# Kernel tuning notes

Hardware: AMD Instinct MI355X
Metric: run time of the kernel (lower is better)

The kernel has to match this reference:

```python
import jax, jax.numpy as jnp
import numpy as np

B, N, M, C = 8, 76725, 32, 12  # N = 9 anchors x (80^2+40^2+20^2+10^2+5^2) for a 640x640 image, P3-P7
IMG = 640.0


def setup_inputs() -> dict:
    key = jax.random.key(0)
    ks = jax.random.split(key, 7)
    # logits biased toward prior_prob~0.01 like the head's bias init
    cls_logits = jax.random.normal(ks[0], (B, N, C), jnp.float32) - 4.0
    box_deltas = 0.1 * jax.random.normal(ks[1], (B, N, 4), jnp.float32)
    # plausible anchors: random centers in image, sizes 16..256
    a_xy = jax.random.uniform(ks[2], (N, 2), jnp.float32) * IMG
    a_wh = 16.0 + jax.random.uniform(ks[3], (N, 2), jnp.float32) * 240.0
    anchors = jnp.concatenate([a_xy - 0.5 * a_wh, a_xy + 0.5 * a_wh], axis=-1)
    # padded ground truth: M boxes per image, all valid
    g_xy = jax.random.uniform(ks[4], (B, M, 2), jnp.float32) * (IMG - 96.0)
    g_wh = 16.0 + jax.random.uniform(ks[5], (B, M, 2), jnp.float32) * 80.0
    gt_boxes = jnp.concatenate([g_xy, g_xy + g_wh], axis=-1)
    gt_labels = jax.random.randint(ks[6], (B, M), 0, C)
    gt_valid = jnp.ones((B, M), dtype=bool)
    return {"cls_logits": cls_logits, "box_deltas": box_deltas, "anchors": anchors,
            "gt_boxes": gt_boxes, "gt_labels": gt_labels, "gt_valid": gt_valid}


def _box_iou(anchors, gt_boxes):
    # anchors [N,4], gt_boxes [B,M,4] -> [B,N,M]
    ax1, ay1, ax2, ay2 = (anchors[:, i] for i in range(4))
    gx1, gy1, gx2, gy2 = (gt_boxes[..., i] for i in range(4))
    iw = jnp.clip(jnp.minimum(ax2[None, :, None], gx2[:, None, :])
                  - jnp.maximum(ax1[None, :, None], gx1[:, None, :]), 0.0)
    ih = jnp.clip(jnp.minimum(ay2[None, :, None], gy2[:, None, :])
                  - jnp.maximum(ay1[None, :, None], gy1[:, None, :]), 0.0)
    inter = iw * ih
    area_a = (ax2 - ax1) * (ay2 - ay1)            # [N]
    area_g = (gx2 - gx1) * (gy2 - gy1)            # [B,M]
    union = area_a[None, :, None] + area_g[:, None, :] - inter
    return inter / union


def _encode_boxes(anchors, matched):
    aw = anchors[:, 2] - anchors[:, 0]
    ah = anchors[:, 3] - anchors[:, 1]
    acx = anchors[:, 0] + 0.5 * aw
    acy = anchors[:, 1] + 0.5 * ah
    gw = matched[..., 2] - matched[..., 0]
    gh = matched[..., 3] - matched[..., 1]
    gcx = matched[..., 0] + 0.5 * gw
    gcy = matched[..., 1] + 0.5 * gh
    return jnp.stack([(gcx - acx) / aw, (gcy - acy) / ah,
                      jnp.log(gw / aw), jnp.log(gh / ah)], axis=-1)


def reference(cls_logits, box_deltas, anchors, gt_boxes, gt_labels, gt_valid):
    # --- anchor assignment (box_iou + max over GT) ---
    ious = _box_iou(anchors, gt_boxes)                       # [B,N,M]
    ious = jnp.where(gt_valid[:, None, :], ious, -1.0)
    iou_max = ious.max(axis=-1)                              # [B,N]
    idx = ious.argmax(axis=-1)                               # [B,N]
    pos = iou_max >= 0.5
    valid = pos | (iou_max < 0.4)                            # non-ignore anchors
    matched = jnp.take_along_axis(
        gt_boxes, jnp.broadcast_to(idx[:, :, None], (B, N, 4)), axis=1)  # [B,N,4]
    mlab = jnp.take_along_axis(gt_labels, idx, axis=1)       # [B,N]
    f32 = cls_logits.dtype
    cls_t = jax.nn.one_hot(mlab, C, dtype=f32) * pos[..., None].astype(f32)
    # --- sigmoid focal loss (alpha=0.25, gamma=2), mean over non-ignored elements ---
    p = jax.nn.sigmoid(cls_logits)
    ce = -(cls_t * jax.nn.log_sigmoid(cls_logits)
           + (1.0 - cls_t) * jax.nn.log_sigmoid(-cls_logits))
    pt = cls_t * p + (1.0 - cls_t) * (1.0 - p)
    alpha_t = cls_t * 0.25 + (1.0 - cls_t) * 0.75
    focal = alpha_t * (1.0 - pt) ** 2 * ce                   # [B,N,C]
    vw = valid.astype(f32)
    cls_loss = jnp.sum(focal * vw[..., None]) / jnp.maximum(jnp.sum(vw) * C, 1.0)
    # --- smooth L1 (beta=1) on positives, mean over selected elements ---
    box_t = _encode_boxes(anchors, matched)                  # [B,N,4]
    d = jnp.abs(box_deltas - box_t)
    sl1 = jnp.where(d < 1.0, 0.5 * d * d, d - 0.5)
    pw = pos.astype(f32)
    box_loss = jnp.sum(sl1 * pw[..., None]) / jnp.maximum(jnp.sum(pw) * 4.0, 1.0)
    return cls_loss + box_loss
```

## Files before the change

### kernel.cpp

```cpp
#include <hip/hip_runtime.h>
#include <math.h>

#define NB 8
#define NA 76725
#define NM 32
#define NC 12
#define BLK 256
#define GX  128
#define NBLOCKS (GX * NB)


__global__ __launch_bounds__(BLK) void retina_fused(
    const float* __restrict__ cls_logits,
    const float* __restrict__ box_deltas,
    const float* __restrict__ anchors,
    const float* __restrict__ gt_boxes,
    const int* __restrict__ gt_labels,
    char* __restrict__ ws,
    int nslots, int slot_stride,
    unsigned int* __restrict__ cnt,
    float* __restrict__ out)
{
    __shared__ float4 s_gt[NM];
    __shared__ float  s_area[NM];
    __shared__ int    s_lab[NM];
    __shared__ int    s_islast;
    __shared__ double s_acc[64][4];

    const int b   = blockIdx.y;
    const int tid = threadIdx.x;

    if (tid < NM) {
        float4 g = ((const float4*)gt_boxes)[b * NM + tid];
        s_gt[tid]   = g;
        s_area[tid] = (g.z - g.x) * (g.w - g.y);
        s_lab[tid]  = gt_labels[b * NM + tid];
    }
    __syncthreads();

    float fsum = 0.0f;
    float ssum = 0.0f;
    int   vcnt = 0;
    int   pcnt = 0;

    for (int n0 = blockIdx.x * BLK; n0 < NA; n0 += GX * BLK) {
        const int n = n0 + tid;
        if (n >= NA) break;

        const float4 a = ((const float4*)anchors)[n];
        const float area_a = (a.z - a.x) * (a.w - a.y);

        float b_inter, b_uni;
        int   bidx = 0;
        {
            const float4 g = s_gt[0];
            const float iw = fmaxf(fminf(a.z, g.z) - fmaxf(a.x, g.x), 0.0f);
            const float ih = fmaxf(fminf(a.w, g.w) - fmaxf(a.y, g.y), 0.0f);
            b_inter = iw * ih;
            b_uni   = (area_a + s_area[0]) - b_inter;
        }
        #pragma unroll
        for (int m = 1; m < NM; ++m) {
            const float4 g = s_gt[m];
            const float iw = fmaxf(fminf(a.z, g.z) - fmaxf(a.x, g.x), 0.0f);
            const float ih = fmaxf(fminf(a.w, g.w) - fmaxf(a.y, g.y), 0.0f);
            const float inter = iw * ih;
            const float uni   = (area_a + s_area[m]) - inter;
            const bool gt = inter * b_uni > b_inter * uni;
            b_inter = gt ? inter : b_inter;
            b_uni   = gt ? uni   : b_uni;
            bidx    = gt ? m     : bidx;
        }

        const bool pos   = (b_inter >= 0.5f * b_uni);
        const bool valid = pos || (b_inter < 0.4f * b_uni);
        vcnt += valid ? 1 : 0;
        pcnt += pos ? 1 : 0;

        if (valid) {
            const int lab = pos ? s_lab[bidx] : -1;
            const float4* cl =
                (const float4*)(cls_logits + ((size_t)b * NA + n) * NC);
            float x[NC];
            const float4 c0 = cl[0], c1 = cl[1], c2 = cl[2];
            x[0]=c0.x; x[1]=c0.y; x[2]=c0.z; x[3]=c0.w;
            x[4]=c1.x; x[5]=c1.y; x[6]=c1.z; x[7]=c1.w;
            x[8]=c2.x; x[9]=c2.y; x[10]=c2.z; x[11]=c2.w;
            #pragma unroll
            for (int c = 0; c < NC; ++c) {
                const float xx = x[c];
                const float ax = fabsf(xx);
                const float e  = __expf(-ax);
                const float t  = 1.0f + e;
                const float l1pe = __logf(t);
                const float u  = __builtin_amdgcn_rcpf(t);
                const float v  = e * u;
                const bool xpos = (xx >= 0.0f);
                const float sp_mx = l1pe + fmaxf(-xx, 0.0f);
                const float sp_px = l1pe + fmaxf(xx, 0.0f);
                const bool tgt = (c == lab);
                const float q = tgt ? (xpos ? v : u) : (xpos ? u : v);
                const float s = tgt ? sp_mx : sp_px;
                const float al = tgt ? 0.25f : 0.75f;
                fsum += al * q * q * s;
            }
        }

        if (pos) {
            const float4 g = s_gt[bidx];
            const float aw  = a.z - a.x;
            const float ah  = a.w - a.y;
            const float r_aw = __builtin_amdgcn_rcpf(aw);
            const float r_ah = __builtin_amdgcn_rcpf(ah);
            const float acx = a.x + 0.5f * aw;
            const float acy = a.y + 0.5f * ah;
            const float gw  = g.z - g.x;
            const float gh  = g.w - g.y;
            const float gcx = g.x + 0.5f * gw;
            const float gcy = g.y + 0.5f * gh;
            const float t0 = (gcx - acx) * r_aw;
            const float t1 = (gcy - acy) * r_ah;
            const float t2 = __logf(gw * r_aw);
            const float t3 = __logf(gh * r_ah);
            const float4 d4 =
                ((const float4*)box_deltas)[(size_t)b * NA + n];
            float d;
            d = fabsf(d4.x - t0); ssum += (d < 1.0f) ? 0.5f * d * d : d - 0.5f;
            d = fabsf(d4.y - t1); ssum += (d < 1.0f) ? 0.5f * d * d : d - 0.5f;
            d = fabsf(d4.z - t2); ssum += (d < 1.0f) ? 0.5f * d * d : d - 0.5f;
            d = fabsf(d4.w - t3); ssum += (d < 1.0f) ? 0.5f * d * d : d - 0.5f;
        }
    }

    float4 v = make_float4(fsum, ssum, (float)vcnt, (float)pcnt);
    #pragma unroll
    for (int off = 32; off > 0; off >>= 1) {
        v.x += __shfl_down(v.x, off);
        v.y += __shfl_down(v.y, off);
        v.z += __shfl_down(v.z, off);
        v.w += __shfl_down(v.w, off);
    }
    __shared__ float4 s_red[BLK / 64];
    const int wave = tid >> 6;
    const int lane = tid & 63;
    if (lane == 0) s_red[wave] = v;
    __syncthreads();

    if (tid == 0) {
        float4 t = s_red[0];
        #pragma unroll
        for (int w = 1; w < BLK / 64; ++w) {
            t.x += s_red[w].x; t.y += s_red[w].y;
            t.z += s_red[w].z; t.w += s_red[w].w;
        }
        const int slot = (blockIdx.y * GX + blockIdx.x) & (nslots - 1);
        double* a = (double*)(ws + (size_t)slot * slot_stride);
        atomicAdd(&a[0], (double)t.x);
        atomicAdd(&a[1], (double)t.y);
        atomicAdd(&a[2], (double)t.z);
        atomicAdd(&a[3], (double)t.w);
        __threadfence();
        const unsigned int old = atomicAdd(cnt, 1u);
        s_islast = (old == NBLOCKS - 1) ? 1 : 0;
    }
    __syncthreads();

    if (s_islast) {
        __threadfence();
        if (tid < nslots) {
            const double* a = (const double*)(ws + (size_t)tid * slot_stride);
            #pragma unroll
            for (int j = 0; j < 4; ++j)
                s_acc[tid][j] = __hip_atomic_load(&a[j], __ATOMIC_RELAXED,
                                                  __HIP_MEMORY_SCOPE_AGENT);
        }
        __syncthreads();
        if (tid == 0) {
            double fs = 0.0, ss = 0.0, vc = 0.0, pc = 0.0;
            for (int k = 0; k < nslots; ++k) {
                fs += s_acc[k][0]; ss += s_acc[k][1];
                vc += s_acc[k][2]; pc += s_acc[k][3];
            }
            const double cls_loss = fs / fmax(vc * (double)NC, 1.0);
            const double box_loss = ss / fmax(pc * 4.0, 1.0);
            out[0] = (float)(cls_loss + box_loss);
        }
    }
}

extern "C" void kernel_launch(void* const* d_in, const int* in_sizes, int n_in,
                              void* d_out, int out_size, void* d_ws, size_t ws_size,
                              hipStream_t stream) {
    const float* cls_logits = (const float*)d_in[0];
    const float* box_deltas = (const float*)d_in[1];
    const float* anchors    = (const float*)d_in[2];
    const float* gt_boxes   = (const float*)d_in[3];
    const int*   gt_labels  = (const int*)d_in[4];
    float* out = (float*)d_out;

    int nslots, stride;
    if (ws_size >= (size_t)(64 * 64 + 8)) { nslots = 64; stride = 64; }
    else                                  { nslots = 1;  stride = 32; }
    unsigned int* cnt = (unsigned int*)((char*)d_ws + (size_t)nslots * stride);

    hipMemsetAsync(d_ws, 0, (size_t)nslots * stride + 8, stream);
    dim3 grid(GX, NB);
    retina_fused<<<grid, BLK, 0, stream>>>(
        cls_logits, box_deltas, anchors, gt_boxes, gt_labels,
        (char*)d_ws, nslots, stride, cnt, out);
}
```

Baseline: 122.2 us.

## Use one anchor per thread with full grid and prefetch logits before IoU

Drops the grid-stride loop and launches one block per 256 anchors per image (300x8 blocks instead of 128x8). The anchor and classification logits loads are issued up front, before the shared-memory setup and IoU loop, so memory latency overlaps with compute. This trades more blocks, and so more atomics on the 64 slots and the counter, for more memory-level parallelism. Logits are now loaded even for ignored anchors.

```diff
diff --git a/kernel.cpp b/kernel.cpp
--- a/kernel.cpp
+++ b/kernel.cpp
@@ -6,8 +6,8 @@
 #define NM 32
 #define NC 12
 #define BLK 256
-#define GX  128
-#define NBLOCKS (GX * NB)
+#define NBLK_X ((NA + BLK - 1) / BLK)
+#define NBLOCKS (NBLK_X * NB)
 
 
 __global__ __launch_bounds__(BLK) void retina_fused(
@@ -25,10 +25,19 @@
     __shared__ float  s_area[NM];
     __shared__ int    s_lab[NM];
     __shared__ int    s_islast;
-    __shared__ double s_acc[64][4];
 
     const int b   = blockIdx.y;
     const int tid = threadIdx.x;
+    const int n   = blockIdx.x * BLK + tid;
+    const bool live = (n < NA);
+
+    float4 a  = make_float4(0.f, 0.f, 1.f, 1.f);
+    float4 c0 = make_float4(0.f, 0.f, 0.f, 0.f), c1 = c0, c2 = c0;
+    if (live) {
+        a = ((const float4*)anchors)[n];
+        const float4* cl = (const float4*)(cls_logits + ((size_t)b * NA + n) * NC);
+        c0 = cl[0]; c1 = cl[1]; c2 = cl[2];
+    }
 
     if (tid < NM) {
         float4 g = ((const float4*)gt_boxes)[b * NM + tid];
@@ -43,11 +52,7 @@
     int   vcnt = 0;
     int   pcnt = 0;
 
-    for (int n0 = blockIdx.x * BLK; n0 < NA; n0 += GX * BLK) {
-        const int n = n0 + tid;
-        if (n >= NA) break;
-
-        const float4 a = ((const float4*)anchors)[n];
+    if (live) {
         const float area_a = (a.z - a.x) * (a.w - a.y);
 
         float b_inter, b_uni;
@@ -74,15 +79,12 @@
 
         const bool pos   = (b_inter >= 0.5f * b_uni);
         const bool valid = pos || (b_inter < 0.4f * b_uni);
-        vcnt += valid ? 1 : 0;
-        pcnt += pos ? 1 : 0;
+        vcnt = valid ? 1 : 0;
+        pcnt = pos ? 1 : 0;
 
         if (valid) {
             const int lab = pos ? s_lab[bidx] : -1;
-            const float4* cl =
-                (const float4*)(cls_logits + ((size_t)b * NA + n) * NC);
             float x[NC];
-            const float4 c0 = cl[0], c1 = cl[1], c2 = cl[2];
             x[0]=c0.x; x[1]=c0.y; x[2]=c0.z; x[3]=c0.w;
             x[4]=c1.x; x[5]=c1.y; x[6]=c1.z; x[7]=c1.w;
             x[8]=c2.x; x[9]=c2.y; x[10]=c2.z; x[11]=c2.w;
@@ -153,12 +155,12 @@
             t.x += s_red[w].x; t.y += s_red[w].y;
             t.z += s_red[w].z; t.w += s_red[w].w;
         }
-        const int slot = (blockIdx.y * GX + blockIdx.x) & (nslots - 1);
-        double* a = (double*)(ws + (size_t)slot * slot_stride);
-        atomicAdd(&a[0], (double)t.x);
-        atomicAdd(&a[1], (double)t.y);
-        atomicAdd(&a[2], (double)t.z);
-        atomicAdd(&a[3], (double)t.w);
+        const int slot = (blockIdx.y * NBLK_X + blockIdx.x) & (nslots - 1);
+        double* acc = (double*)(ws + (size_t)slot * slot_stride);
+        atomicAdd(&acc[0], (double)t.x);
+        atomicAdd(&acc[1], (double)t.y);
+        atomicAdd(&acc[2], (double)t.z);
+        atomicAdd(&acc[3], (double)t.w);
         __threadfence();
         const unsigned int old = atomicAdd(cnt, 1u);
         s_islast = (old == NBLOCKS - 1) ? 1 : 0;
@@ -167,11 +169,12 @@
 
     if (s_islast) {
         __threadfence();
+        __shared__ double s_acc[64][4];
         if (tid < nslots) {
-            const double* a = (const double*)(ws + (size_t)tid * slot_stride);
+            const double* acc = (const double*)(ws + (size_t)tid * slot_stride);
             #pragma unroll
             for (int j = 0; j < 4; ++j)
-                s_acc[tid][j] = __hip_atomic_load(&a[j], __ATOMIC_RELAXED,
+                s_acc[tid][j] = __hip_atomic_load(&acc[j], __ATOMIC_RELAXED,
                                                   __HIP_MEMORY_SCOPE_AGENT);
         }
         __syncthreads();
@@ -204,7 +207,7 @@
     unsigned int* cnt = (unsigned int*)((char*)d_ws + (size_t)nslots * stride);
 
     hipMemsetAsync(d_ws, 0, (size_t)nslots * stride + 8, stream);
-    dim3 grid(GX, NB);
+    dim3 grid(NBLK_X, NB);
     retina_fused<<<grid, BLK, 0, stream>>>(
         cls_logits, box_deltas, anchors, gt_boxes, gt_labels,
         (char*)d_ws, nslots, stride, cnt, out);
```

Measured after the change: 152.5 us. 1.25x slower.

## Hoist logits loads before IoU loop and use two-level completion counter

Applied to the files above, without the earlier changes.

The classification logits for each anchor are now loaded unconditionally before the IoU matching loop, so memory latency overlaps the 32-box compute. The cost is extra bandwidth for ignored anchors, whose logits were skipped before. Completion detection moves from one global counter to per-slot counters plus a second-level counter, to spread atomic contention. Launch bounds now request 4 blocks per CU, and the small-workspace fallback is removed, which assumes the workspace is large enough.

```diff
diff --git a/kernel.cpp b/kernel.cpp
--- a/kernel.cpp
+++ b/kernel.cpp
@@ -8,24 +8,24 @@
 #define BLK 256
 #define GX  128
 #define NBLOCKS (GX * NB)
-
-
-__global__ __launch_bounds__(BLK) void retina_fused(
+#define NSLOTS 64
+#define QUOTA (NBLOCKS / NSLOTS)
+
+
+__global__ __launch_bounds__(BLK, 4) void retina_fused(
     const float* __restrict__ cls_logits,
     const float* __restrict__ box_deltas,
     const float* __restrict__ anchors,
     const float* __restrict__ gt_boxes,
     const int* __restrict__ gt_labels,
     char* __restrict__ ws,
-    int nslots, int slot_stride,
-    unsigned int* __restrict__ cnt,
+    unsigned int* __restrict__ cnt2,
     float* __restrict__ out)
 {
     __shared__ float4 s_gt[NM];
     __shared__ float  s_area[NM];
     __shared__ int    s_lab[NM];
     __shared__ int    s_islast;
-    __shared__ double s_acc[64][4];
 
     const int b   = blockIdx.y;
     const int tid = threadIdx.x;
@@ -48,6 +48,9 @@
         if (n >= NA) break;
 
         const float4 a = ((const float4*)anchors)[n];
+        const float4* cl = (const float4*)(cls_logits + ((size_t)b * NA + n) * NC);
+        const float4 c0 = cl[0], c1 = cl[1], c2 = cl[2];
+
         const float area_a = (a.z - a.x) * (a.w - a.y);
 
         float b_inter, b_uni;
@@ -79,10 +82,7 @@
 
         if (valid) {
             const int lab = pos ? s_lab[bidx] : -1;
-            const float4* cl =
-                (const float4*)(cls_logits + ((size_t)b * NA + n) * NC);
             float x[NC];
-            const float4 c0 = cl[0], c1 = cl[1], c2 = cl[2];
             x[0]=c0.x; x[1]=c0.y; x[2]=c0.z; x[3]=c0.w;
             x[4]=c1.x; x[5]=c1.y; x[6]=c1.z; x[7]=c1.w;
             x[8]=c2.x; x[9]=c2.y; x[10]=c2.z; x[11]=c2.w;
@@ -153,31 +153,40 @@
             t.x += s_red[w].x; t.y += s_red[w].y;
             t.z += s_red[w].z; t.w += s_red[w].w;
         }
-        const int slot = (blockIdx.y * GX + blockIdx.x) & (nslots - 1);
-        double* a = (double*)(ws + (size_t)slot * slot_stride);
-        atomicAdd(&a[0], (double)t.x);
-        atomicAdd(&a[1], (double)t.y);
-        atomicAdd(&a[2], (double)t.z);
-        atomicAdd(&a[3], (double)t.w);
+        const int flat = blockIdx.y * GX + blockIdx.x;
+        const int slot = flat & (NSLOTS - 1);
+        double* acc = (double*)(ws + (size_t)slot * 64);
+        atomicAdd(&acc[0], (double)t.x);
+        atomicAdd(&acc[1], (double)t.y);
+        atomicAdd(&acc[2], (double)t.z);
+        atomicAdd(&acc[3], (double)t.w);
         __threadfence();
-        const unsigned int old = atomicAdd(cnt, 1u);
-        s_islast = (old == NBLOCKS - 1) ? 1 : 0;
+        unsigned int* slot_cnt = (unsigned int*)(ws + (size_t)slot * 64 + 32);
+        const unsigned int old = atomicAdd(slot_cnt, 1u);
+        int islast = 0;
+        if (old == QUOTA - 1) {
+            __threadfence();
+            const unsigned int o2 = atomicAdd(cnt2, 1u);
+            islast = (o2 == NSLOTS - 1) ? 1 : 0;
+        }
+        s_islast = islast;
     }
     __syncthreads();
 
     if (s_islast) {
         __threadfence();
-        if (tid < nslots) {
-            const double* a = (const double*)(ws + (size_t)tid * slot_stride);
+        __shared__ double s_acc[NSLOTS][4];
+        if (tid < NSLOTS) {
+            const double* acc = (const double*)(ws + (size_t)tid * 64);
             #pragma unroll
             for (int j = 0; j < 4; ++j)
-                s_acc[tid][j] = __hip_atomic_load(&a[j], __ATOMIC_RELAXED,
+                s_acc[tid][j] = __hip_atomic_load(&acc[j], __ATOMIC_RELAXED,
                                                   __HIP_MEMORY_SCOPE_AGENT);
         }
         __syncthreads();
         if (tid == 0) {
             double fs = 0.0, ss = 0.0, vc = 0.0, pc = 0.0;
-            for (int k = 0; k < nslots; ++k) {
+            for (int k = 0; k < NSLOTS; ++k) {
                 fs += s_acc[k][0]; ss += s_acc[k][1];
                 vc += s_acc[k][2]; pc += s_acc[k][3];
             }
@@ -198,14 +207,12 @@
     const int*   gt_labels  = (const int*)d_in[4];
     float* out = (float*)d_out;
 
-    int nslots, stride;
-    if (ws_size >= (size_t)(64 * 64 + 8)) { nslots = 64; stride = 64; }
-    else                                  { nslots = 1;  stride = 32; }
-    unsigned int* cnt = (unsigned int*)((char*)d_ws + (size_t)nslots * stride);
-
-    hipMemsetAsync(d_ws, 0, (size_t)nslots * stride + 8, stream);
+    char* ws = (char*)d_ws;
+    unsigned int* cnt2 = (unsigned int*)(ws + (size_t)NSLOTS * 64);
+
+    hipMemsetAsync(d_ws, 0, (size_t)NSLOTS * 64 + 4, stream);
     dim3 grid(GX, NB);
     retina_fused<<<grid, BLK, 0, stream>>>(
         cls_logits, box_deltas, anchors, gt_boxes, gt_labels,
-        (char*)d_ws, nslots, stride, cnt, out);
+        ws, cnt2, out);
 }
```

Result: slower. 180.7 us (+47.8%).
